# Performance work log

Hardware: AMD Instinct MI355X
Metric: run time of the kernel (lower is better)

## Reference

```python
import jax, jax.numpy as jnp
import numpy as np

B, L, D, H = 2, 2048, 1024, 16
DH = D // H
LN_EPS = 1e-5


def setup_inputs() -> dict:
    key = jax.random.key(0)
    ks = jax.random.split(key, 6)
    s = 1.0 / np.sqrt(D)
    return {
        "x": jax.random.normal(ks[0], (B, L, D), dtype=jnp.float32),
        "market_info": jax.random.uniform(ks[1], (B, 8), dtype=jnp.float32),
        "in_proj_w": jax.random.normal(ks[2], (3 * D, D), dtype=jnp.float32) * s,
        "in_proj_b": jnp.zeros((3 * D,), dtype=jnp.float32),
        "out_proj_w": jax.random.normal(ks[3], (D, D), dtype=jnp.float32) * s,
        "out_proj_b": jnp.zeros((D,), dtype=jnp.float32),
        "ln_gamma": jnp.ones((D,), dtype=jnp.float32),
        "ln_beta": jnp.zeros((D,), dtype=jnp.float32),
    }


def reference(x, market_info, in_proj_w, in_proj_b, out_proj_w, out_proj_b, ln_gamma, ln_beta):
    # fused QKV projection (torch nn.MultiheadAttention in_proj)
    qkv = jnp.einsum("bld,ed->ble", x, in_proj_w) + in_proj_b  # (B,L,3D)
    q, k, v = jnp.split(qkv, 3, axis=-1)
    q = q.reshape(B, L, H, DH)
    k = k.reshape(B, L, H, DH)
    v = v.reshape(B, L, H, DH)
    scale = 1.0 / jnp.sqrt(jnp.asarray(DH, dtype=x.dtype))
    scores = jnp.einsum("blhd,bmhd->bhlm", q, k) * scale  # (B,H,L,L)
    # market mask: per-batch volatility scalar added to every score
    vol = market_info[:, 0][:, None, None, None]  # (B,1,1,1)
    attn = jax.nn.softmax(scores + vol, axis=-1)
    ctx = jnp.einsum("bhlm,bmhd->blhd", attn, v).reshape(B, L, D)
    attended = jnp.einsum("bld,ed->ble", ctx, out_proj_w) + out_proj_b
    # residual + LayerNorm (dropout=0 / eval)
    y = x + attended
    mu = jnp.mean(y, axis=-1, keepdims=True)
    var = jnp.mean(jnp.square(y - mu), axis=-1, keepdims=True)
    return (y - mu) * jax.lax.rsqrt(var + LN_EPS) * ln_gamma + ln_beta
```

## Files before the change

### kernel.cpp

```cpp
#include <hip/hip_runtime.h>
#include <math.h>

#define B_  2
#define L_  2048
#define D_  1024
#define H_  16
#define DH_ 64
#define E3D 3072
#define LN_EPS 1e-5f

typedef unsigned short u16;
typedef __attribute__((ext_vector_type(8))) short bf16x8;
typedef __attribute__((ext_vector_type(4))) float f32x4;

__device__ inline unsigned pack2(float lo, float hi) {
    unsigned a = __builtin_bit_cast(unsigned, lo) + 0x8000u;
    unsigned b = __builtin_bit_cast(unsigned, hi) + 0x8000u;
    return __builtin_amdgcn_perm(b, a, 0x07060302);
}
__device__ inline unsigned pack2t(float lo, float hi) {
    return __builtin_amdgcn_perm(__builtin_bit_cast(unsigned, hi),
                                 __builtin_bit_cast(unsigned, lo), 0x07060302);
}
__device__ inline float bf2f(u16 v) {
    return __builtin_bit_cast(float, (unsigned)v << 16);
}
__device__ inline void async16(const void* g, void* l) {
    __builtin_amdgcn_global_load_lds(
        (const __attribute__((address_space(1))) unsigned*)g,
        (__attribute__((address_space(3))) unsigned*)l, 16, 0, 0);
}

#define QSCALE (0.125f * 1.44269504088896f)

__global__ __launch_bounds__(256) void cvt_all(
    const float* __restrict__ x, const float* __restrict__ iw,
    const float* __restrict__ ow, u16* __restrict__ xb,
    u16* __restrict__ iwb, u16* __restrict__ owb)
{
    const int bid = blockIdx.x;
    const float* src; u16* dst; int base;
    if (bid < 2048)      { src = x;  dst = xb;  base = bid * 2048; }
    else if (bid < 3584) { src = iw; dst = iwb; base = (bid - 2048) * 2048; }
    else                 { src = ow; dst = owb; base = (bid - 3584) * 2048; }
    const int i = base + threadIdx.x * 8;
    float4 v0 = *(const float4*)(src + i);
    float4 v1 = *(const float4*)(src + i + 4);
    uint4 w;
    w.x = pack2(v0.x, v0.y); w.y = pack2(v0.z, v0.w);
    w.z = pack2(v1.x, v1.y); w.w = pack2(v1.z, v1.w);
    *(uint4*)(dst + i) = w;
}

template<int MT>
__global__ __launch_bounds__(256) void gemm_bf16(
    const u16* __restrict__ A, const u16* __restrict__ W,
    const float* __restrict__ bias, u16* __restrict__ outB,
    int M, int N, int K, int qlimit)
{
    constexpr int WC  = (MT == 128) ? 4 : 2;
    constexpr int STG = (MT + 128) * 64 * 2;
    constexpr int EPI = MT * 68 * 4;
    constexpr int SMEMB = (STG > EPI) ? STG : EPI;
    __shared__ __align__(16) char smem[SMEMB];
    u16* As0 = (u16*)smem;
    u16* As1 = As0 + MT * 32;
    u16* Ws0 = As1 + MT * 32;
    u16* Ws1 = Ws0 + 128 * 32;

    const int t    = threadIdx.x;
    const int wave = t >> 6;
    const int lane = t & 63;
    const int a    = lane & 15;
    const int g    = lane >> 4;
    const int row0 = blockIdx.y * MT;
    const int col0 = blockIdx.x * 128;

    const int srowA = wave * (MT / 4) + (lane >> 2);
    const int srowW = wave * 32 + (lane >> 2);
    const int sseg  = (lane & 3) * 8;
    const u16* Ag = A + (size_t)(row0 + srowA) * K + sseg;
    const u16* Wg = W + (size_t)(col0 + srowW) * K + sseg;
    u16* As0W = &As0[wave * (MT / 4) * 32];
    u16* As1W = &As1[wave * (MT / 4) * 32];
    u16* Ws0W = &Ws0[wave * 32 * 32];
    u16* Ws1W = &Ws1[wave * 32 * 32];

    f32x4 acc[4][WC];
    #pragma unroll
    for (int i = 0; i < 4; ++i)
        #pragma unroll
        for (int j = 0; j < WC; ++j)
            acc[i][j] = (f32x4){0.f, 0.f, 0.f, 0.f};

    const int ar = (MT == 128) ? (wave & 1) * 64 : 0;
    const int wc = (MT == 128) ? (wave >> 1) * 64 : wave * 32;

    for (int kt = 0; kt < K; kt += 64) {
        __syncthreads();
        if (MT == 128) {
            async16(Ag + kt,                       As0W);
            async16(Ag + (size_t)16 * K + kt,      As0W + 16 * 32);
            async16(Ag + kt + 32,                  As1W);
            async16(Ag + (size_t)16 * K + kt + 32, As1W + 16 * 32);
        } else {
            async16(Ag + kt,      As0W);
            async16(Ag + kt + 32, As1W);
        }
        async16(Wg + kt,                       Ws0W);
        async16(Wg + (size_t)16 * K + kt,      Ws0W + 16 * 32);
        async16(Wg + kt + 32,                  Ws1W);
        async16(Wg + (size_t)16 * K + kt + 32, Ws1W + 16 * 32);
        __syncthreads();

        bf16x8 af[4][2], wf[WC][2];
        #pragma unroll
        for (int i = 0; i < 4; ++i) {
            af[i][0] = *(const bf16x8*)&As0[(ar + i * 16 + a) * 32 + g * 8];
            af[i][1] = *(const bf16x8*)&As1[(ar + i * 16 + a) * 32 + g * 8];
        }
        #pragma unroll
        for (int j = 0; j < WC; ++j) {
            wf[j][0] = *(const bf16x8*)&Ws0[(wc + j * 16 + a) * 32 + g * 8];
            wf[j][1] = *(const bf16x8*)&Ws1[(wc + j * 16 + a) * 32 + g * 8];
        }
        #pragma unroll
        for (int i = 0; i < 4; ++i)
            #pragma unroll
            for (int j = 0; j < WC; ++j) {
                acc[i][j] = __builtin_amdgcn_mfma_f32_16x16x32_bf16(
                    wf[j][0], af[i][0], acc[i][j], 0, 0, 0);
                acc[i][j] = __builtin_amdgcn_mfma_f32_16x16x32_bf16(
                    wf[j][1], af[i][1], acc[i][j], 0, 0, 0);
            }
    }

    const float s = (col0 < qlimit) ? QSCALE : 1.0f;
    __syncthreads();
    unsigned* Cs = (unsigned*)smem;
    #pragma unroll
    for (int j = 0; j < WC; ++j) {
        const int cb = wc + j * 16 + g * 4;
        const float4 bj = *(const float4*)(bias + col0 + cb);
        #pragma unroll
        for (int i = 0; i < 4; ++i) {
            const int row = ar + i * 16 + a;
            uint2 w;
            w.x = pack2((acc[i][j][0] + bj.x) * s, (acc[i][j][1] + bj.y) * s);
            w.y = pack2((acc[i][j][2] + bj.z) * s, (acc[i][j][3] + bj.w) * s);
            *(uint2*)&Cs[row * 68 + (cb >> 1)] = w;
        }
    }
    __syncthreads();
    #pragma unroll
    for (int p = 0; p < MT / 16; ++p) {
        const int rowX = (MT == 128) ? ((t >> 2) + (p & 1) * 64) : (t >> 2);
        const int c2X  = (MT == 128) ? ((t & 3) * 4 + (p >> 1) * 16)
                                     : ((t & 3) * 4 + p * 16);
        uint4 w = *(const uint4*)&Cs[rowX * 68 + c2X];
        *(uint4*)&outB[(size_t)(row0 + rowX) * N + col0 + c2X * 2] = w;
    }
}

__global__ __launch_bounds__(256) void attn_mfma(
    const u16* __restrict__ qkv, u16* __restrict__ Oun, float* __restrict__ lbuf)
{
    const int bid  = blockIdx.x;
    const int v_   = ((bid & 7) << 7) | (bid >> 3);
    const int half = v_ >> 9;
    const int rest = v_ & 511;
    const int qt   = rest & 15;
    const int bh   = rest >> 4;
    const int h    = bh & 15;
    const int b    = bh >> 4;
    const int qb0  = qt * 128;

    const int t    = threadIdx.x;
    const int wave = t >> 6;
    const int lane = t & 63;
    const int a    = lane & 15;
    const int g    = lane >> 4;

    __shared__ __align__(16) u16 Kt[64 * 72];
    __shared__ __align__(16) u16 VtT[80 * 72];
    __shared__ __align__(16) u16 Pl[4 * 2 * 16 * 72];

    for (int idx = t; idx < 16 * 36; idx += 256) {
        const int r = idx / 36;
        const int w = idx - r * 36;
        ((unsigned*)VtT)[(64 + r) * 36 + w] = (r == 0) ? 0x3F803F80u : 0u;
    }

    bf16x8 qf[2][2];
    #pragma unroll
    for (int q2 = 0; q2 < 2; ++q2) {
        const u16* qrow = qkv + (size_t)(b * L_ + qb0 + wave * 32 + q2 * 16 + a) * E3D
                        + h * DH_;
        #pragma unroll
        for (int c = 0; c < 2; ++c)
            qf[q2][c] = *(const bf16x8*)(qrow + c * 32 + g * 8);
    }

    __syncthreads();
    bf16x8 onesf[2];
    #pragma unroll
    for (int c = 0; c < 2; ++c)
        onesf[c] = *(const bf16x8*)&VtT[(64 + a) * 72 + c * 32 + g * 8];

    f32x4 o[2][4];
    f32x4 l4[2];
    #pragma unroll
    for (int q2 = 0; q2 < 2; ++q2) {
        #pragma unroll
        for (int dt = 0; dt < 4; ++dt)
            o[q2][dt] = (f32x4){0.f, 0.f, 0.f, 0.f};
        l4[q2] = (f32x4){0.f, 0.f, 0.f, 0.f};
    }

    const int krow = t >> 2;
    const int kseg = (t & 3) * 16;
    const int vu   = t >> 3;
    const int vc8  = (t & 7) * 8;
    const int vj0  = t & 7;

    const u16* kbase = qkv + (size_t)(b * L_) * E3D + D_ + h * DH_;
    const u16* vbase = qkv + (size_t)(b * L_) * E3D + 2 * D_ + h * DH_;

    const int k_lo = half * (L_ / 2);
    const int k_hi = k_lo + L_ / 2;

    uint4 kx0, kx1, va, vb;
    {
        const u16* kr = kbase + (size_t)(k_lo + krow) * E3D + kseg;
        kx0 = *(const uint4*)kr;
        kx1 = *(const uint4*)(kr + 8);
        const u16* vr = vbase + (size_t)(k_lo + 2 * vu) * E3D + vc8;
        va = *(const uint4*)vr;
        vb = *(const uint4*)(vr + E3D);
    }

    for (int k0 = k_lo; k0 < k_hi; k0 += 64) {
        __syncthreads();

        *(uint4*)&Kt[krow * 72 + kseg]     = kx0;
        *(uint4*)&Kt[krow * 72 + kseg + 8] = kx1;
        {
            const unsigned av[4] = {va.x, va.y, va.z, va.w};
            const unsigned bv[4] = {vb.x, vb.y, vb.z, vb.w};
            unsigned* Vw = (unsigned*)VtT;
            #pragma unroll
            for (int i = 0; i < 8; ++i) {
                const int j = (i + vj0) & 7;
                const unsigned xa = av[j >> 1], xb = bv[j >> 1];
                const unsigned v = (j & 1) ? ((xa >> 16) | (xb & 0xffff0000u))
                                           : ((xa & 0xffffu) | (xb << 16));
                Vw[(vc8 + j) * 36 + vu] = v;
            }
        }
        __syncthreads();

        if (k0 + 64 < k_hi) {
            const u16* kr = kbase + (size_t)(k0 + 64 + krow) * E3D + kseg;
            kx0 = *(const uint4*)kr;
            kx1 = *(const uint4*)(kr + 8);
            const u16* vr = vbase + (size_t)(k0 + 64 + 2 * vu) * E3D + vc8;
            va = *(const uint4*)vr;
            vb = *(const uint4*)(vr + E3D);
        }

        f32x4 s[2][4];
        #pragma unroll
        for (int q2 = 0; q2 < 2; ++q2)
            #pragma unroll
            for (int kt = 0; kt < 4; ++kt)
                s[q2][kt] = (f32x4){0.f, 0.f, 0.f, 0.f};
        #pragma unroll
        for (int kt = 0; kt < 4; ++kt) {
            bf16x8 kf0 = *(const bf16x8*)&Kt[(kt * 16 + a) * 72 + g * 8];
            bf16x8 kf1 = *(const bf16x8*)&Kt[(kt * 16 + a) * 72 + 32 + g * 8];
            #pragma unroll
            for (int q2 = 0; q2 < 2; ++q2) {
                s[q2][kt] = __builtin_amdgcn_mfma_f32_16x16x32_bf16(kf0, qf[q2][0], s[q2][kt], 0, 0, 0);
                s[q2][kt] = __builtin_amdgcn_mfma_f32_16x16x32_bf16(kf1, qf[q2][1], s[q2][kt], 0, 0, 0);
            }
        }

        #pragma unroll
        for (int q2 = 0; q2 < 2; ++q2) {
            unsigned* Pw = (unsigned*)&Pl[(wave * 2 + q2) * (16 * 72)];
            #pragma unroll
            for (int kt = 0; kt < 4; ++kt) {
                const float p0 = __builtin_amdgcn_exp2f(s[q2][kt][0]);
                const float p1 = __builtin_amdgcn_exp2f(s[q2][kt][1]);
                const float p2 = __builtin_amdgcn_exp2f(s[q2][kt][2]);
                const float p3 = __builtin_amdgcn_exp2f(s[q2][kt][3]);
                uint2 w;
                w.x = pack2t(p0, p1);
                w.y = pack2t(p2, p3);
                *(uint2*)&Pw[a * 36 + kt * 8 + g * 2] = w;
            }
        }

        #pragma unroll
        for (int c = 0; c < 2; ++c) {
            bf16x8 pf[2];
            #pragma unroll
            for (int q2 = 0; q2 < 2; ++q2)
                pf[q2] = *(const bf16x8*)&Pl[(wave * 2 + q2) * (16 * 72) + a * 72 + c * 32 + g * 8];
            #pragma unroll
            for (int dt = 0; dt < 4; ++dt) {
                bf16x8 vf = *(const bf16x8*)&VtT[(dt * 16 + a) * 72 + c * 32 + g * 8];
                #pragma unroll
                for (int q2 = 0; q2 < 2; ++q2)
                    o[q2][dt] = __builtin_amdgcn_mfma_f32_16x16x32_bf16(vf, pf[q2], o[q2][dt], 0, 0, 0);
            }
            #pragma unroll
            for (int q2 = 0; q2 < 2; ++q2)
                l4[q2] = __builtin_amdgcn_mfma_f32_16x16x32_bf16(onesf[c], pf[q2], l4[q2], 0, 0, 0);
        }
    }

    #pragma unroll
    for (int q2 = 0; q2 < 2; ++q2) {
        const int qrow = qb0 + wave * 32 + q2 * 16 + a;
        const size_t row = (size_t)(b * L_ + qrow);
        if (g == 0)
            lbuf[(size_t)half * 65536 + row * 16 + h] = l4[q2][0];
        u16* cp = Oun + (size_t)half * 4096 * 1024 + row * D_ + h * DH_;
        #pragma unroll
        for (int dt = 0; dt < 4; ++dt) {
            uint2 w;
            w.x = pack2(o[q2][dt][0], o[q2][dt][1]);
            w.y = pack2(o[q2][dt][2], o[q2][dt][3]);
            *(uint2*)&cp[dt * 16 + g * 4] = w;
        }
    }
}

__global__ __launch_bounds__(256) void attn_merge(
    const u16* __restrict__ Oun, const float* __restrict__ lbuf,
    u16* __restrict__ ctx)
{
    const int row = blockIdx.x;
    const int t   = threadIdx.x;
    const int col = t * 4;
    const int h   = col >> 6;
    const float inv = 1.f / (lbuf[(size_t)row * 16 + h] +
                             lbuf[(size_t)65536 + row * 16 + h]);
    const size_t base = (size_t)row * D_ + col;
    uint2 w0 = *(const uint2*)&Oun[base];
    uint2 w1 = *(const uint2*)&Oun[(size_t)4096 * 1024 + base];
    float f0 = (bf2f((u16)(w0.x & 0xffff)) + bf2f((u16)(w1.x & 0xffff))) * inv;
    float f1 = (bf2f((u16)(w0.x >> 16))    + bf2f((u16)(w1.x >> 16)))    * inv;
    float f2 = (bf2f((u16)(w0.y & 0xffff)) + bf2f((u16)(w1.y & 0xffff))) * inv;
    float f3 = (bf2f((u16)(w0.y >> 16))    + bf2f((u16)(w1.y >> 16)))    * inv;
    uint2 w;
    w.x = pack2(f0, f1);
    w.y = pack2(f2, f3);
    *(uint2*)&ctx[base] = w;
}

__global__ __launch_bounds__(256) void ln_rows(
    const float* __restrict__ x, const u16* __restrict__ att,
    const float* __restrict__ gamma, const float* __restrict__ beta,
    float* __restrict__ out)
{
    const int row = blockIdx.x;
    const int t = threadIdx.x;
    const size_t base = (size_t)row * D_ + t * 4;

    float4 v = *(const float4*)(x + base);
    uint2 aw = *(const uint2*)(att + base);
    v.x += bf2f((u16)(aw.x & 0xffff));
    v.y += bf2f((u16)(aw.x >> 16));
    v.z += bf2f((u16)(aw.y & 0xffff));
    v.w += bf2f((u16)(aw.y >> 16));

    float s  = v.x + v.y + v.z + v.w;
    float s2 = v.x * v.x + v.y * v.y + v.z * v.z + v.w * v.w;
    #pragma unroll
    for (int off = 32; off > 0; off >>= 1) {
        s  += __shfl_down(s, off);
        s2 += __shfl_down(s2, off);
    }
    __shared__ float red[4], red2[4];
    const int wid = t >> 6, lid = t & 63;
    if (lid == 0) { red[wid] = s; red2[wid] = s2; }
    __syncthreads();
    if (t == 0) {
        float aa = 0.f, b2 = 0.f;
        #pragma unroll
        for (int i = 0; i < 4; ++i) { aa += red[i]; b2 += red2[i]; }
        red[0] = aa; red2[0] = b2;
    }
    __syncthreads();
    const float mu   = red[0] * (1.f / D_);
    const float var  = red2[0] * (1.f / D_) - mu * mu;
    const float rstd = rsqrtf(var + LN_EPS);

    float4 gm = *(const float4*)(gamma + t * 4);
    float4 bt = *(const float4*)(beta + t * 4);
    float4 oo;
    oo.x = (v.x - mu) * rstd * gm.x + bt.x;
    oo.y = (v.y - mu) * rstd * gm.y + bt.y;
    oo.z = (v.z - mu) * rstd * gm.z + bt.z;
    oo.w = (v.w - mu) * rstd * gm.w + bt.w;
    *(float4*)(out + base) = oo;
}

extern "C" void kernel_launch(void* const* d_in, const int* in_sizes, int n_in,
                              void* d_out, int out_size, void* d_ws, size_t ws_size,
                              hipStream_t stream)
{
    const float* x      = (const float*)d_in[0];
    const float* in_w   = (const float*)d_in[2];
    const float* in_b   = (const float*)d_in[3];
    const float* out_w  = (const float*)d_in[4];
    const float* out_b  = (const float*)d_in[5];
    const float* gamma  = (const float*)d_in[6];
    const float* beta   = (const float*)d_in[7];
    float* out = (float*)d_out;

    char* ws   = (char*)d_ws;
    u16*  qkvb = (u16*)ws;
    u16*  Oun  = (u16*)(ws + 25165824);
    u16*  po   = (u16*)(ws + 25165824);
    u16*  ctxb = (u16*)(ws + 41943040);
    u16*  xb   = (u16*)(ws + 50331648);
    float* lb  = (float*)(ws + 50331648);
    u16*  iwb  = (u16*)(ws + 58720256);
    u16*  owb  = (u16*)(ws + 65011712);

    dim3 blk(256);
    cvt_all<<<dim3(4096), blk, 0, stream>>>(x, in_w, out_w, xb, iwb, owb);

    gemm_bf16<128><<<dim3(E3D / 128, (B_ * L_) / 128), blk, 0, stream>>>(
        xb, iwb, in_b, qkvb, B_ * L_, E3D, D_, D_);

    attn_mfma<<<dim3(2 * B_ * H_ * (L_ / 128)), blk, 0, stream>>>(qkvb, Oun, lb);
    attn_merge<<<dim3(B_ * L_), blk, 0, stream>>>(Oun, lb, ctxb);

    gemm_bf16<64><<<dim3(D_ / 128, (B_ * L_) / 64), blk, 0, stream>>>(
        ctxb, owb, out_b, po, B_ * L_, D_, D_, 0);

    ln_rows<<<dim3(B_ * L_), blk, 0, stream>>>(x, po, gamma, beta, out);
}
```

Baseline: 208.8 us.

## Write V transposed from the QKV GEMM epilogue to drop in-attention transpose

Measured after the change: 212.3 us. Within noise of the previous version (+1.7%).

```diff
diff --git a/kernel.cpp b/kernel.cpp
--- a/kernel.cpp
+++ b/kernel.cpp
@@ -13,6 +13,9 @@
 typedef __attribute__((ext_vector_type(8))) short bf16x8;
 typedef __attribute__((ext_vector_type(4))) float f32x4;
 
+__device__ inline u16 f2bf(float x) {
+    return (u16)((__builtin_bit_cast(unsigned, x) + 0x8000u) >> 16);
+}
 __device__ inline unsigned pack2(float lo, float hi) {
     unsigned a = __builtin_bit_cast(unsigned, lo) + 0x8000u;
     unsigned b = __builtin_bit_cast(unsigned, hi) + 0x8000u;
@@ -52,11 +55,11 @@
     *(uint4*)(dst + i) = w;
 }
 
-template<int MT>
+template<int MT, int MODE>
 __global__ __launch_bounds__(256) void gemm_bf16(
     const u16* __restrict__ A, const u16* __restrict__ W,
     const float* __restrict__ bias, u16* __restrict__ outB,
-    int M, int N, int K, int qlimit)
+    u16* __restrict__ vTo, int M, int N, int K, int qlimit)
 {
     constexpr int WC  = (MT == 128) ? 4 : 2;
     constexpr int STG = (MT + 128) * 64 * 2;
@@ -135,8 +138,39 @@
             }
     }
 
+    __syncthreads();
+
+    if (MODE == 1 && MT == 128 && col0 >= 2048) {
+        u16* Cs16 = (u16*)smem;
+        #pragma unroll
+        for (int j = 0; j < WC; ++j) {
+            const int cbase = wc + j * 16 + g * 4;
+            const float4 bj = *(const float4*)(bias + col0 + cbase);
+            #pragma unroll
+            for (int i = 0; i < 4; ++i) {
+                const int row = ar + i * 16 + a;
+                Cs16[(cbase + 0) * 136 + row] = f2bf(acc[i][j][0] + bj.x);
+                Cs16[(cbase + 1) * 136 + row] = f2bf(acc[i][j][1] + bj.y);
+                Cs16[(cbase + 2) * 136 + row] = f2bf(acc[i][j][2] + bj.z);
+                Cs16[(cbase + 3) * 136 + row] = f2bf(acc[i][j][3] + bj.w);
+            }
+        }
+        __syncthreads();
+        const int bb   = row0 >> 11;
+        const int key0 = row0 & 2047;
+        const int hd0  = col0 - 2048;
+        #pragma unroll
+        for (int p = 0; p < 8; ++p) {
+            const int ccX = (t >> 2) + (p & 1) * 64;
+            const int c2X = (t & 3) * 4 + (p >> 1) * 16;
+            uint4 w = *(const uint4*)&((unsigned*)smem)[ccX * 68 + c2X];
+            *(uint4*)&vTo[(size_t)(bb * 1024 + hd0 + ccX) * 2048 + key0 + c2X * 2] = w;
+        }
+        return;
+    }
+
+    const int NS = (MODE == 1) ? 2048 : N;
     const float s = (col0 < qlimit) ? QSCALE : 1.0f;
-    __syncthreads();
     unsigned* Cs = (unsigned*)smem;
     #pragma unroll
     for (int j = 0; j < WC; ++j) {
@@ -158,12 +192,13 @@
         const int c2X  = (MT == 128) ? ((t & 3) * 4 + (p >> 1) * 16)
                                      : ((t & 3) * 4 + p * 16);
         uint4 w = *(const uint4*)&Cs[rowX * 68 + c2X];
-        *(uint4*)&outB[(size_t)(row0 + rowX) * N + col0 + c2X * 2] = w;
+        *(uint4*)&outB[(size_t)(row0 + rowX) * NS + col0 + c2X * 2] = w;
     }
 }
 
 __global__ __launch_bounds__(256) void attn_mfma(
-    const u16* __restrict__ qkv, u16* __restrict__ Oun, float* __restrict__ lbuf)
+    const u16* __restrict__ qk, const u16* __restrict__ vT,
+    u16* __restrict__ Oun, float* __restrict__ lbuf)
 {
     const int bid  = blockIdx.x;
     const int v_   = ((bid & 7) << 7) | (bid >> 3);
@@ -194,7 +229,7 @@
     bf16x8 qf[2][2];
     #pragma unroll
     for (int q2 = 0; q2 < 2; ++q2) {
-        const u16* qrow = qkv + (size_t)(b * L_ + qb0 + wave * 32 + q2 * 16 + a) * E3D
+        const u16* qrow = qk + (size_t)(b * L_ + qb0 + wave * 32 + q2 * 16 + a) * 2048
                         + h * DH_;
         #pragma unroll
         for (int c = 0; c < 2; ++c)
@@ -219,53 +254,39 @@
 
     const int krow = t >> 2;
     const int kseg = (t & 3) * 16;
-    const int vu   = t >> 3;
-    const int vc8  = (t & 7) * 8;
-    const int vj0  = t & 7;
-
-    const u16* kbase = qkv + (size_t)(b * L_) * E3D + D_ + h * DH_;
-    const u16* vbase = qkv + (size_t)(b * L_) * E3D + 2 * D_ + h * DH_;
+
+    const u16* kbase = qk + (size_t)(b * L_) * 2048 + 1024 + h * DH_;
+    const u16* vrowb = vT + (size_t)(b * 1024 + h * DH_ + krow) * 2048;
 
     const int k_lo = half * (L_ / 2);
     const int k_hi = k_lo + L_ / 2;
 
-    uint4 kx0, kx1, va, vb;
+    uint4 kx0, kx1, vx0, vx1;
     {
-        const u16* kr = kbase + (size_t)(k_lo + krow) * E3D + kseg;
+        const u16* kr = kbase + (size_t)(k_lo + krow) * 2048 + kseg;
         kx0 = *(const uint4*)kr;
         kx1 = *(const uint4*)(kr + 8);
-        const u16* vr = vbase + (size_t)(k_lo + 2 * vu) * E3D + vc8;
-        va = *(const uint4*)vr;
-        vb = *(const uint4*)(vr + E3D);
+        const u16* vr = vrowb + k_lo + kseg;
+        vx0 = *(const uint4*)vr;
+        vx1 = *(const uint4*)(vr + 8);
     }
 
     for (int k0 = k_lo; k0 < k_hi; k0 += 64) {
         __syncthreads();
 
-        *(uint4*)&Kt[krow * 72 + kseg]     = kx0;
-        *(uint4*)&Kt[krow * 72 + kseg + 8] = kx1;
-        {
-            const unsigned av[4] = {va.x, va.y, va.z, va.w};
-            const unsigned bv[4] = {vb.x, vb.y, vb.z, vb.w};
-            unsigned* Vw = (unsigned*)VtT;
-            #pragma unroll
-            for (int i = 0; i < 8; ++i) {
-                const int j = (i + vj0) & 7;
-                const unsigned xa = av[j >> 1], xb = bv[j >> 1];
-                const unsigned v = (j & 1) ? ((xa >> 16) | (xb & 0xffff0000u))
-                                           : ((xa & 0xffffu) | (xb << 16));
-                Vw[(vc8 + j) * 36 + vu] = v;
-            }
-        }
+        *(uint4*)&Kt[krow * 72 + kseg]      = kx0;
+        *(uint4*)&Kt[krow * 72 + kseg + 8]  = kx1;
+        *(uint4*)&VtT[krow * 72 + kseg]     = vx0;
+        *(uint4*)&VtT[krow * 72 + kseg + 8] = vx1;
         __syncthreads();
 
         if (k0 + 64 < k_hi) {
-            const u16* kr = kbase + (size_t)(k0 + 64 + krow) * E3D + kseg;
+            const u16* kr = kbase + (size_t)(k0 + 64 + krow) * 2048 + kseg;
             kx0 = *(const uint4*)kr;
             kx1 = *(const uint4*)(kr + 8);
-            const u16* vr = vbase + (size_t)(k0 + 64 + 2 * vu) * E3D + vc8;
-            va = *(const uint4*)vr;
-            vb = *(const uint4*)(vr + E3D);
+            const u16* vr = vrowb + k0 + 64 + kseg;
+            vx0 = *(const uint4*)vr;
+            vx1 = *(const uint4*)(vr + 8);
         }
 
         f32x4 s[2][4];
@@ -422,7 +443,8 @@
     float* out = (float*)d_out;
 
     char* ws   = (char*)d_ws;
-    u16*  qkvb = (u16*)ws;
+    u16*  qkb  = (u16*)ws;
+    u16*  vTb  = (u16*)(ws + 16777216);
     u16*  Oun  = (u16*)(ws + 25165824);
     u16*  po   = (u16*)(ws + 25165824);
     u16*  ctxb = (u16*)(ws + 41943040);
@@ -434,14 +456,14 @@
     dim3 blk(256);
     cvt_all<<<dim3(4096), blk, 0, stream>>>(x, in_w, out_w, xb, iwb, owb);
 
-    gemm_bf16<128><<<dim3(E3D / 128, (B_ * L_) / 128), blk, 0, stream>>>(
-        xb, iwb, in_b, qkvb, B_ * L_, E3D, D_, D_);
-
-    attn_mfma<<<dim3(2 * B_ * H_ * (L_ / 128)), blk, 0, stream>>>(qkvb, Oun, lb);
+    gemm_bf16<128, 1><<<dim3(E3D / 128, (B_ * L_) / 128), blk, 0, stream>>>(
+        xb, iwb, in_b, qkb, vTb, B_ * L_, E3D, D_, D_);
+
+    attn_mfma<<<dim3(2 * B_ * H_ * (L_ / 128)), blk, 0, stream>>>(qkb, vTb, Oun, lb);
     attn_merge<<<dim3(B_ * L_), blk, 0, stream>>>(Oun, lb, ctxb);
 
-    gemm_bf16<64><<<dim3(D_ / 128, (B_ * L_) / 64), blk, 0, stream>>>(
-        ctxb, owb, out_b, po, B_ * L_, D_, D_, 0);
+    gemm_bf16<64, 0><<<dim3(D_ / 128, (B_ * L_) / 64), blk, 0, stream>>>(
+        ctxb, owb, out_b, po, nullptr, B_ * L_, D_, D_, 0);
 
     ln_rows<<<dim3(B_ * L_), blk, 0, stream>>>(x, po, gamma, beta, out);
 }
```
